# Kernel tuning notes

Hardware: AMD Instinct MI355X
Metric: run time of the kernel (lower is better)

The kernel has to match this reference:

```python
import jax, jax.numpy as jnp
import numpy as np

CUTOFF = 5.0
EMB = 64
RAD = 32
N_ATOMS = 20000
N_SPECIES = 100
N_EDGES = 200000


def setup_inputs() -> dict:
    key = jax.random.key(0)
    k = jax.random.split(key, 8)
    Z = jax.random.randint(k[0], (N_ATOMS,), 0, N_SPECIES)
    neighbour_index = jax.random.randint(k[1], (N_EDGES, 2), 0, N_ATOMS)
    # random 3D offsets; norm ~1.6 << cutoff so envelope is active
    neighbour_vectors = jax.random.normal(k[2], (N_EDGES, 3), dtype=jnp.float32)
    z_embed = jax.random.normal(k[3], (N_SPECIES, EMB), dtype=jnp.float32) * 0.1
    z_map_w = jax.random.normal(k[4], (EMB, 2 * EMB), dtype=jnp.float32) / np.sqrt(2 * EMB)
    r_map_w = jax.random.normal(k[5], (3 * EMB, RAD), dtype=jnp.float32) / np.sqrt(RAD)
    r_map_b = jax.random.normal(k[6], (3 * EMB,), dtype=jnp.float32) * 0.01
    # PhysNet-style exponential RBF: centers in (exp(-cutoff), 1], fixed width
    rbf_centers = jnp.linspace(np.exp(-CUTOFF), 1.0, RAD, dtype=jnp.float32)
    beta_val = ((2.0 / RAD) * (1.0 - np.exp(-CUTOFF))) ** -2
    rbf_betas = jnp.full((RAD,), beta_val, dtype=jnp.float32)
    return {
        "Z": Z,
        "neighbour_index": neighbour_index,
        "neighbour_vectors": neighbour_vectors,
        "z_embed": z_embed,
        "z_map_w": z_map_w,
        "r_map_w": r_map_w,
        "r_map_b": r_map_b,
        "rbf_centers": rbf_centers,
        "rbf_betas": rbf_betas,
    }


def _edge_embedding(Z, neighbour_index, neighbour_vectors, z_embed,
                    z_map_w, r_map_w, r_map_b, rbf_centers, rbf_betas):
    r = jnp.linalg.norm(neighbour_vectors, axis=-1)          # [E]
    r_hat = neighbour_vectors / r[:, None]                   # [E,3]

    # initial geometric tensors
    x, y, z = r_hat[:, 0], r_hat[:, 1], r_hat[:, 2]
    zero = jnp.zeros_like(x)
    A0 = jnp.stack([zero, -z, y,
                    z, zero, -x,
                    -y, x, zero], axis=1).reshape(-1, 3, 3)   # [E,3,3] skew
    outer = r_hat[:, :, None] * r_hat[:, None, :]             # [E,3,3]
    tr_mean = (outer[:, 0, 0] + outer[:, 1, 1] + outer[:, 2, 2]) / 3.0
    eye3 = jnp.eye(3, dtype=neighbour_vectors.dtype)
    S0 = outer - tr_mean[:, None, None] * eye3                # symmetric, traceless

    # species embedding per edge: concat(embed(z_i) || embed(z_j)) -> linear (no bias)
    h_z_atom = z_embed[Z]                                     # [N,emb]
    h_z_edge = h_z_atom[neighbour_index].reshape(-1, 2 * EMB)  # [E,2emb]
    h_z_edge = h_z_edge @ z_map_w.T                           # [E,emb]

    # exponential radial basis + cosine envelope
    expansion = jnp.exp(-rbf_betas * (jnp.exp(-r)[:, None] - rbf_centers) ** 2)  # [E,rad]
    env = jnp.where(r < CUTOFF, 0.5 * (jnp.cos(jnp.pi * r / CUTOFF) + 1.0), 0.0)  # [E]

    c = (expansion @ r_map_w.T + r_map_b) * env[:, None] * jnp.tile(h_z_edge, (1, 3))  # [E,3emb]
    c_I, c_A, c_S = jnp.split(c, 3, axis=1)                   # each [E,emb]

    out_I = c_I[:, :, None, None] * eye3                       # [E,emb,3,3]
    out_A = c_A[:, :, None, None] * A0[:, None, :, :]
    out_S = c_S[:, :, None, None] * S0[:, None, :, :]
    return out_I, out_A, out_S


def reference(Z, neighbour_index, neighbour_vectors, z_embed,
              z_map_w, r_map_w, r_map_b, rbf_centers, rbf_betas):
    return _edge_embedding(Z, neighbour_index, neighbour_vectors, z_embed,
                           z_map_w, r_map_w, r_map_b, rbf_centers, rbf_betas)
```

## Files before the change

### kernel.cpp

```cpp
#include <hip/hip_runtime.h>

#define EMB 64
#define RAD 32
#define CUTOFF_F 5.0f

typedef float f32x4 __attribute__((ext_vector_type(4)));

__global__ void species_proj_kernel(const float* __restrict__ z_embed,
                                    const float* __restrict__ z_map_w,
                                    float* __restrict__ pA,
                                    float* __restrict__ pB) {
    const int s = blockIdx.x;
    const int k = threadIdx.x;
    const float* ze = z_embed + s * EMB;
    const float* wk = z_map_w + k * (2 * EMB);
    float a = 0.f, b = 0.f;
#pragma unroll 8
    for (int j = 0; j < EMB; ++j) {
        const float e = ze[j];
        a = fmaf(e, wk[j], a);
        b = fmaf(e, wk[EMB + j], b);
    }
    pA[s * EMB + k] = a;
    pB[s * EMB + k] = b;
}

__global__ __launch_bounds__(256) void edge_embed_kernel(
    const int* __restrict__ Z,
    const int* __restrict__ nbr,
    const float* __restrict__ nv,
    const float* __restrict__ rmw,
    const float* __restrict__ rmb,
    const float* __restrict__ rbfc,
    const float* __restrict__ rbfb,
    const float* __restrict__ pA,
    const float* __restrict__ pB,
    float* __restrict__ out,
    int E) {
    __shared__ __align__(16) float buf[4][3 * EMB * 9];

    const int tid  = threadIdx.x;
    const int w    = tid >> 6;
    const int lane = tid & 63;

    float W0[RAD], W1[RAD], W2[RAD];
#pragma unroll
    for (int j = 0; j < RAD; ++j) {
        W0[j] = rmw[lane * RAD + j];
        W1[j] = rmw[(lane + EMB) * RAD + j];
        W2[j] = rmw[(lane + 2 * EMB) * RAD + j];
    }
    const float b0 = rmb[lane], b1 = rmb[lane + EMB], b2 = rmb[lane + 2 * EMB];
    const float cj = rbfc[lane & (RAD - 1)];
    const float bj = rbfb[lane & (RAD - 1)];

    float* bw = buf[w];
    {
        const int o = lane * 9;
        bw[o + 1] = 0.f; bw[o + 2] = 0.f; bw[o + 3] = 0.f;
        bw[o + 5] = 0.f; bw[o + 6] = 0.f; bw[o + 7] = 0.f;
        bw[576 + o + 0] = 0.f; bw[576 + o + 4] = 0.f; bw[576 + o + 8] = 0.f;
    }

    const size_t strideT = (size_t)E * (EMB * 9);
    const int gw = blockIdx.x * 4 + w;
    const int nw = gridDim.x * 4;

    for (int e0 = gw; e0 < E; e0 += nw) {
        const int e = __builtin_amdgcn_readfirstlane(e0);

        const int   i0 = nbr[2 * e], i1 = nbr[2 * e + 1];
        const float vx = nv[3 * e], vy = nv[3 * e + 1], vz = nv[3 * e + 2];
        const int   s0 = Z[i0], s1 = Z[i1];

        const float r2   = vx * vx + vy * vy + vz * vz;
        const float r    = sqrtf(r2);
        const float rinv = 1.0f / r;
        const float x = vx * rinv, y = vy * rinv, z = vz * rinv;

        float env = 0.f;
        if (r < CUTOFF_F)
            env = 0.5f * (cosf((3.14159265358979f / CUTOFF_F) * r) + 1.0f);

        const float t = expf(-r);
        const float d = t - cj;
        const float g = expf(-bj * d * d);

        const float h = pA[s0 * EMB + lane] + pB[s1 * EMB + lane];

        float aI = b0, aA = b1, aS = b2;
#pragma unroll
        for (int j = 0; j < RAD; ++j) {
            const float gj =
                __int_as_float(__builtin_amdgcn_readlane(__float_as_int(g), j));
            aI = fmaf(gj, W0[j], aI);
            aA = fmaf(gj, W1[j], aA);
            aS = fmaf(gj, W2[j], aS);
        }
        const float eh = env * h;
        const float cI = aI * eh, cA = aA * eh, cS = aS * eh;

        const int o = lane * 9;
        bw[o + 0] = cI; bw[o + 4] = cI; bw[o + 8] = cI;

        bw[576 + o + 1] = -z * cA; bw[576 + o + 2] =  y * cA;
        bw[576 + o + 3] =  z * cA; bw[576 + o + 5] = -x * cA;
        bw[576 + o + 6] = -y * cA; bw[576 + o + 7] =  x * cA;

        const float m = (x * x + y * y + z * z) * (1.f / 3.f);
        bw[1152 + o + 0] = (x * x - m) * cS;
        bw[1152 + o + 1] = x * y * cS;
        bw[1152 + o + 2] = x * z * cS;
        bw[1152 + o + 3] = x * y * cS;
        bw[1152 + o + 4] = (y * y - m) * cS;
        bw[1152 + o + 5] = y * z * cS;
        bw[1152 + o + 6] = x * z * cS;
        bw[1152 + o + 7] = y * z * cS;
        bw[1152 + o + 8] = (z * z - m) * cS;

        __builtin_amdgcn_sched_barrier(0);

        const size_t ebase = (size_t)e * (EMB * 9);
#pragma unroll
        for (int ts = 0; ts < 3; ++ts) {
#pragma unroll
            for (int i = 0; i < 3; ++i) {
                const int q = lane + (i << 6);
                if (q < 144) {
                    const f32x4 v =
                        *reinterpret_cast<const f32x4*>(bw + ts * 576 + 4 * q);
                    __builtin_nontemporal_store(
                        v, reinterpret_cast<f32x4*>(out + strideT * ts + ebase + 4 * q));
                }
            }
        }
        __builtin_amdgcn_sched_barrier(0);
    }
}

extern "C" void kernel_launch(void* const* d_in, const int* in_sizes, int n_in,
                              void* d_out, int out_size, void* d_ws, size_t ws_size,
                              hipStream_t stream) {
    const int*   Z       = (const int*)d_in[0];
    const int*   nbr     = (const int*)d_in[1];
    const float* nv      = (const float*)d_in[2];
    const float* z_embed = (const float*)d_in[3];
    const float* z_map_w = (const float*)d_in[4];
    const float* rmw     = (const float*)d_in[5];
    const float* rmb     = (const float*)d_in[6];
    const float* rbfc    = (const float*)d_in[7];
    const float* rbfb    = (const float*)d_in[8];
    float*       out     = (float*)d_out;

    const int E         = in_sizes[2] / 3;
    const int n_species = in_sizes[3] / EMB;

    float* pA = (float*)d_ws;
    float* pB = pA + (size_t)n_species * EMB;

    species_proj_kernel<<<n_species, EMB, 0, stream>>>(z_embed, z_map_w, pA, pB);
    edge_embed_kernel<<<1024, 256, 0, stream>>>(Z, nbr, nv, rmw, rmb, rbfc, rbfb,
                                                pA, pB, out, E);
}
```

Before: 289.8 us.

## Software-pipeline per-edge gathers and use fast intrinsics in edge kernel

```diff
diff --git a/kernel.cpp b/kernel.cpp
--- a/kernel.cpp
+++ b/kernel.cpp
@@ -63,30 +63,41 @@
     }
 
     const size_t strideT = (size_t)E * (EMB * 9);
-    const int gw = blockIdx.x * 4 + w;
     const int nw = gridDim.x * 4;
+    int e = __builtin_amdgcn_readfirstlane(blockIdx.x * 4 + w);
+    if (e >= E) return;
 
-    for (int e0 = gw; e0 < E; e0 += nw) {
-        const int e = __builtin_amdgcn_readfirstlane(e0);
+    int   i0 = nbr[2 * e], i1 = nbr[2 * e + 1];
+    float vx = nv[3 * e], vy = nv[3 * e + 1], vz = nv[3 * e + 2];
+    int   s0 = Z[i0], s1 = Z[i1];
+    float hA = pA[s0 * EMB + lane], hB = pB[s1 * EMB + lane];
 
-        const int   i0 = nbr[2 * e], i1 = nbr[2 * e + 1];
-        const float vx = nv[3 * e], vy = nv[3 * e + 1], vz = nv[3 * e + 2];
-        const int   s0 = Z[i0], s1 = Z[i1];
+    while (true) {
+        const int  en   = __builtin_amdgcn_readfirstlane(e + nw);
+        const bool more = en < E;
+
+        int ni0 = 0, ni1 = 0;
+        float nvx = 0.f, nvy = 0.f, nvz = 0.f;
+        if (more) {
+            ni0 = nbr[2 * en]; ni1 = nbr[2 * en + 1];
+            nvx = nv[3 * en]; nvy = nv[3 * en + 1]; nvz = nv[3 * en + 2];
+        }
 
         const float r2   = vx * vx + vy * vy + vz * vz;
-        const float r    = sqrtf(r2);
-        const float rinv = 1.0f / r;
+        const float rinv = rsqrtf(r2);
+        const float r    = r2 * rinv;
         const float x = vx * rinv, y = vy * rinv, z = vz * rinv;
 
         float env = 0.f;
         if (r < CUTOFF_F)
-            env = 0.5f * (cosf((3.14159265358979f / CUTOFF_F) * r) + 1.0f);
+            env = 0.5f * (__cosf(0.6283185307f * r) + 1.0f);
 
-        const float t = expf(-r);
+        const float t = __expf(-r);
         const float d = t - cj;
-        const float g = expf(-bj * d * d);
+        const float g = __expf(-bj * d * d);
 
-        const float h = pA[s0 * EMB + lane] + pB[s1 * EMB + lane];
+        int ns0 = 0, ns1 = 0;
+        if (more) { ns0 = Z[ni0]; ns1 = Z[ni1]; }
 
         float aI = b0, aA = b1, aS = b2;
 #pragma unroll
@@ -97,7 +108,11 @@
             aA = fmaf(gj, W1[j], aA);
             aS = fmaf(gj, W2[j], aS);
         }
-        const float eh = env * h;
+
+        float nhA = 0.f, nhB = 0.f;
+        if (more) { nhA = pA[ns0 * EMB + lane]; nhB = pB[ns1 * EMB + lane]; }
+
+        const float eh = env * (hA + hB);
         const float cI = aI * eh, cA = aA * eh, cS = aS * eh;
 
         const int o = lane * 9;
@@ -118,8 +133,6 @@
         bw[1152 + o + 7] = y * z * cS;
         bw[1152 + o + 8] = (z * z - m) * cS;
 
-        __builtin_amdgcn_sched_barrier(0);
-
         const size_t ebase = (size_t)e * (EMB * 9);
 #pragma unroll
         for (int ts = 0; ts < 3; ++ts) {
@@ -134,7 +147,11 @@
                 }
             }
         }
-        __builtin_amdgcn_sched_barrier(0);
+
+        if (!more) break;
+        e = en;
+        vx = nvx; vy = nvy; vz = nvz;
+        hA = nhA; hB = nhB;
     }
 }
 
@@ -159,6 +176,6 @@
     float* pB = pA + (size_t)n_species * EMB;
 
     species_proj_kernel<<<n_species, EMB, 0, stream>>>(z_embed, z_map_w, pA, pB);
-    edge_embed_kernel<<<1024, 256, 0, stream>>>(Z, nbr, nv, rmw, rmb, rbfc, rbfb,
+    edge_embed_kernel<<<2000, 256, 0, stream>>>(Z, nbr, nv, rmw, rmb, rbfc, rbfb,
                                                 pA, pB, out, E);
 }
```

Result: faster. 281.3 us (-2.9%).
